# Optimization experiments

Hardware: AMD Instinct MI355X
Metric: run time of the kernel (lower is better)

## Reference

```python
import jax, jax.numpy as jnp
import numpy as np

B, S, H = 1, 2048, 2048
NH = 16
Q_LORA, KV_LORA = 1536, 512
D_NOPE, D_ROPE, D_V = 128, 64, 128
D_QK = D_NOPE + D_ROPE  # 192
EPS = 1e-6
ROPE_BASE = 10000.0


def setup_inputs() -> dict:
    key = jax.random.key(0)
    ks = jax.random.split(key, 8)
    def lin(k, fan_in, fan_out):
        # nn.Linear default init, stored as [in, out] for x @ W
        bound = 1.0 / np.sqrt(fan_in)
        return jax.random.uniform(k, (fan_in, fan_out), jnp.float32, -bound, bound)
    return {
        "hidden_states": jax.random.normal(ks[0], (B, S, H), jnp.float32),
        "Wqa": lin(ks[1], H, Q_LORA),
        "q_a_ln_w": jnp.ones((Q_LORA,), jnp.float32),
        "Wqb": lin(ks[2], Q_LORA, NH * D_QK),
        "Wkva": lin(ks[3], H, KV_LORA + D_ROPE),
        "kv_a_ln_w": jnp.ones((KV_LORA,), jnp.float32),
        "Wkvb": lin(ks[4], KV_LORA, NH * (D_NOPE + D_V)),
        "Wo": lin(ks[5], NH * D_V, H),
    }


def _rmsnorm(x, w):
    xf = x.astype(jnp.float32)
    var = jnp.mean(xf * xf, axis=-1, keepdims=True)
    return w * (xf * jax.lax.rsqrt(var + EPS)).astype(x.dtype)


def _rotate_half(x):
    x1, x2 = jnp.split(x, 2, axis=-1)
    return jnp.concatenate((-x2, x1), axis=-1)


def _rope_tables(seq_len, dtype=jnp.float32):
    inv_freq = 1.0 / (ROPE_BASE ** (jnp.arange(0, D_ROPE, 2, dtype=jnp.float32) / D_ROPE))
    t = jnp.arange(seq_len, dtype=jnp.float32)
    freqs = jnp.outer(t, inv_freq)                      # [S, D_ROPE/2]
    emb = jnp.concatenate((freqs, freqs), axis=-1)      # [S, D_ROPE]
    return jnp.cos(emb).astype(dtype), jnp.sin(emb).astype(dtype)


def reference(hidden_states, Wqa, q_a_ln_w, Wqb, Wkva, kv_a_ln_w, Wkvb, Wo):
    bsz, q_len, _ = hidden_states.shape
    scale = D_QK ** -0.5

    # Q path: LoRA down -> RMSNorm -> up
    q = _rmsnorm(hidden_states @ Wqa, q_a_ln_w) @ Wqb            # [B,S,NH*D_QK]
    q = q.reshape(bsz, q_len, NH, D_QK).transpose(0, 2, 1, 3)    # [B,NH,S,D_QK]
    q_nope, q_pe = q[..., :D_NOPE], q[..., D_NOPE:]

    # KV path: compressed latent + shared rope key
    ckv = hidden_states @ Wkva                                    # [B,S,KV_LORA+D_ROPE]
    compressed_kv, k_pe = ckv[..., :KV_LORA], ckv[..., KV_LORA:]
    k_pe = k_pe.reshape(bsz, q_len, 1, D_ROPE).transpose(0, 2, 1, 3)  # [B,1,S,D_ROPE]
    kv = _rmsnorm(compressed_kv, kv_a_ln_w) @ Wkvb                # [B,S,NH*(D_NOPE+D_V)]
    kv = kv.reshape(bsz, q_len, NH, D_NOPE + D_V).transpose(0, 2, 1, 3)
    k_nope, v = kv[..., :D_NOPE], kv[..., D_NOPE:]                # [B,NH,S,D_NOPE], [B,NH,S,D_V]

    # decoupled RoPE on the rope sub-dims
    cos, sin = _rope_tables(q_len, hidden_states.dtype)
    cos = cos[None, None]  # [1,1,S,D_ROPE] broadcast over batch & heads
    sin = sin[None, None]
    q_pe = q_pe * cos + _rotate_half(q_pe) * sin
    k_pe = k_pe * cos + _rotate_half(k_pe) * sin                  # [B,1,S,D_ROPE]

    query = jnp.concatenate([q_nope, q_pe], axis=-1)              # [B,NH,S,D_QK]
    key = jnp.concatenate([k_nope, jnp.broadcast_to(k_pe, (bsz, NH, q_len, D_ROPE))], axis=-1)

    attn = jnp.einsum('bhqd,bhkd->bhqk', query, key) * scale      # [B,NH,S,S]
    causal = jnp.triu(jnp.ones((q_len, q_len), bool), k=1)
    attn = jnp.where(causal, -jnp.inf, attn)
    attn = jax.nn.softmax(attn.astype(jnp.float32), axis=-1).astype(query.dtype)

    out = jnp.einsum('bhqk,bhkd->bhqd', attn, v)                  # [B,NH,S,D_V]
    out = out.transpose(0, 2, 1, 3).reshape(bsz, q_len, NH * D_V)
    return out @ Wo                                               # [B,S,H]
```

## Files before the change

kernel.cpp:

```cpp
#include <hip/hip_runtime.h>
#include <hip/hip_bf16.h>
#include <math.h>

#define S_LEN 2048
#define H_DIM 2048
#define NH 16
#define Q_LORA 1536
#define KV_LORA 512
#define D_NOPE 128
#define D_ROPE 64
#define D_V 128
#define D_QK 192

typedef unsigned short ushort_t;
typedef __attribute__((ext_vector_type(8))) short short8;
typedef __attribute__((ext_vector_type(4))) float f32x4;

__device__ __forceinline__ ushort_t f2bf(float f) {
    unsigned int u = __float_as_uint(f);
    u = (u + 0x7FFFu + ((u >> 16) & 1u)) >> 16;
    return (ushort_t)u;
}
__device__ __forceinline__ float bf2f(ushort_t u) {
    return __uint_as_float(((unsigned int)u) << 16);
}

__device__ __forceinline__ void storeC(float* p, float v) { *p = v; }
__device__ __forceinline__ void storeC(ushort_t* p, float v) { *p = f2bf(v); }

__device__ __forceinline__ void gload_lds16(const ushort_t* g, ushort_t* l) {
    __builtin_amdgcn_global_load_lds(
        (const __attribute__((address_space(1))) unsigned int*)(const void*)g,
        (__attribute__((address_space(3))) unsigned int*)(void*)l, 16, 0, 0);
}

__device__ __forceinline__ float dpp_max16(float x) {
    x = fmaxf(x, __int_as_float(__builtin_amdgcn_update_dpp(0, __float_as_int(x), 0xB1, 0xF, 0xF, true)));
    x = fmaxf(x, __int_as_float(__builtin_amdgcn_update_dpp(0, __float_as_int(x), 0x4E, 0xF, 0xF, true)));
    x = fmaxf(x, __int_as_float(__builtin_amdgcn_update_dpp(0, __float_as_int(x), 0x124, 0xF, 0xF, true)));
    x = fmaxf(x, __int_as_float(__builtin_amdgcn_update_dpp(0, __float_as_int(x), 0x128, 0xF, 0xF, true)));
    return x;
}
__device__ __forceinline__ float dpp_sum16(float x) {
    x += __int_as_float(__builtin_amdgcn_update_dpp(0, __float_as_int(x), 0xB1, 0xF, 0xF, true));
    x += __int_as_float(__builtin_amdgcn_update_dpp(0, __float_as_int(x), 0x4E, 0xF, 0xF, true));
    x += __int_as_float(__builtin_amdgcn_update_dpp(0, __float_as_int(x), 0x124, 0xF, 0xF, true));
    x += __int_as_float(__builtin_amdgcn_update_dpp(0, __float_as_int(x), 0x128, 0xF, 0xF, true));
    return x;
}

__device__ __forceinline__ void convT_body(
    const float* __restrict__ W, ushort_t* __restrict__ Wt,
    int K, int N, int n0, int k0, float (*tile)[33])
{
    const int tr = threadIdx.x >> 5, tc = threadIdx.x & 31;
    #pragma unroll
    for (int i = 0; i < 4; ++i) {
        int r = tr + i * 8;
        float v = 0.f;
        if (n0 + tc < N) v = W[(size_t)(k0 + r) * N + n0 + tc];
        tile[r][tc] = v;
    }
    __syncthreads();
    #pragma unroll
    for (int i = 0; i < 4; ++i) {
        int r = tr + i * 8;
        Wt[(size_t)(n0 + r) * K + k0 + tc] = f2bf(tile[tc][r]);
    }
}

__global__ __launch_bounds__(256) void unified_conv(
    const float* __restrict__ hs, ushort_t* __restrict__ hs16,
    const float* __restrict__ Wqa, const float* __restrict__ Wkva,
    const float* __restrict__ Wqb, const float* __restrict__ Wkvb,
    const float* __restrict__ Wo,
    ushort_t* __restrict__ WcatT, ushort_t* __restrict__ WqbT,
    ushort_t* __restrict__ WkvbT, ushort_t* __restrict__ WoT)
{
    __shared__ float tile[32][33];
    int b = blockIdx.x;
    if (b < 4096) {
        int base = (b * 256 + threadIdx.x) * 4;
        float4 v = *(const float4*)(hs + base);
        hs16[base + 0] = f2bf(v.x);
        hs16[base + 1] = f2bf(v.y);
        hs16[base + 2] = f2bf(v.z);
        hs16[base + 3] = f2bf(v.w);
        return;
    }
    b -= 4096;
    const float* W; ushort_t* Wt; int K, N, nbx;
    if (b < 3072)        {            W = Wqa;  Wt = WcatT;                              K = 2048; N = 1536; nbx = 48;  }
    else if (b < 4352)   { b -= 3072; W = Wkva; Wt = WcatT + (size_t)Q_LORA * H_DIM;     K = 2048; N = 576;  nbx = 20;  }
    else if (b < 8960)   { b -= 4352; W = Wqb;  Wt = WqbT;                               K = 1536; N = 3072; nbx = 96;  }
    else if (b < 11008)  { b -= 8960; W = Wkvb; Wt = WkvbT;                              K = 512;  N = 4096; nbx = 128; }
    else                 { b -= 11008; W = Wo;  Wt = WoT;                                K = 2048; N = 2048; nbx = 64;  }
    convT_body(W, Wt, K, N, (b % nbx) * 32, (b / nbx) * 32, tile);
}

__global__ __launch_bounds__(256) void fused_norm_ropek(
    const ushort_t* __restrict__ cat16r, ushort_t* __restrict__ qa16,
    ushort_t* __restrict__ ckv16n, ushort_t* __restrict__ kpe16,
    const float* __restrict__ qlnw, const float* __restrict__ klnw)
{
    __shared__ float red[4];
    const int b = blockIdx.x;
    if (b < 4096) {
        const bool isQ = (b < 2048);
        const int row = isQ ? b : b - 2048;
        const int K = isQ ? Q_LORA : KV_LORA;
        const ushort_t* x = cat16r + (size_t)row * 2176 + (isQ ? 0 : Q_LORA);
        ushort_t* y = (isQ ? qa16 + (size_t)row * Q_LORA : ckv16n + (size_t)row * KV_LORA);
        const float* wv = isQ ? qlnw : klnw;
        float ss = 0.f;
        for (int i = threadIdx.x; i < K; i += 256) { float v = bf2f(x[i]); ss += v * v; }
        #pragma unroll
        for (int off = 32; off > 0; off >>= 1) ss += __shfl_down(ss, off);
        int lane = threadIdx.x & 63, wid = threadIdx.x >> 6;
        if (lane == 0) red[wid] = ss;
        __syncthreads();
        float tot = red[0] + red[1] + red[2] + red[3];
        float rs = rsqrtf(tot / (float)K + 1e-6f);
        for (int i = threadIdx.x; i < K; i += 256)
            y[i] = f2bf(bf2f(x[i]) * rs * wv[i]);
    } else {
        int idx = (b - 4096) * 256 + threadIdx.x;
        if (idx >= S_LEN * 32) return;
        int i = idx & 31;
        int s = idx >> 5;
        float inv = powf(10000.0f, -(2.0f * i) / 64.0f);
        float ang = (float)s * inv;
        float c = cosf(ang), sn = sinf(ang);
        const ushort_t* p = cat16r + (size_t)s * 2176 + Q_LORA + KV_LORA;
        ushort_t* q = kpe16 + (size_t)s * D_ROPE;
        float x1 = bf2f(p[i]), x2 = bf2f(p[i + 32]);
        q[i]      = f2bf(x1 * c - x2 * sn);
        q[i + 32] = f2bf(x2 * c + x1 * sn);
    }
}

__global__ __launch_bounds__(256) void conv_vT_kernel(
    const ushort_t* __restrict__ kv, ushort_t* __restrict__ v16t)
{
    __shared__ ushort_t tile[32][33];
    const int h = blockIdx.z;
    const int s0 = blockIdx.x * 32, d0 = blockIdx.y * 32;
    const int tr = threadIdx.x >> 5, tc = threadIdx.x & 31;
    #pragma unroll
    for (int i = 0; i < 4; ++i) {
        int r = tr + i * 8;
        tile[r][tc] = kv[(size_t)(s0 + r) * 4096 + h * 256 + D_NOPE + d0 + tc];
    }
    __syncthreads();
    #pragma unroll
    for (int i = 0; i < 4; ++i) {
        int r = tr + i * 8;
        v16t[(size_t)h * D_V * S_LEN + (size_t)(d0 + r) * S_LEN + s0 + tc] = tile[tc][r];
    }
}

template <typename CT>
__device__ __forceinline__ void gemm_body_128(
    const ushort_t* __restrict__ A, const ushort_t* __restrict__ Bt,
    CT* __restrict__ C, int N, int K, int m0, int n0,
    ushort_t* Al, ushort_t* Bl)
{
    const int tid = threadIdx.x;
    const int lane = tid & 63;
    const int w = tid >> 6;
    const int lm = lane & 15, quad = lane >> 4;
    const int wr = w >> 1, wc = w & 1;

    f32x4 acc[4][4];
    #pragma unroll
    for (int a = 0; a < 4; ++a)
        #pragma unroll
        for (int b = 0; b < 4; ++b) acc[a][b] = (f32x4){0.f, 0.f, 0.f, 0.f};

    const int rrow = tid >> 2;
    const int rcol = (tid & 3) * 8;

    for (int k0 = 0; k0 < K; k0 += 64) {
        __syncthreads();
        #pragma unroll
        for (int c = 0; c < 2; ++c)
            #pragma unroll
            for (int half = 0; half < 2; ++half) {
                gload_lds16(A + (size_t)(m0 + half * 64 + rrow) * K + k0 + c * 32 + rcol,
                            Al + c * 4096 + half * 2048 + tid * 8);
                gload_lds16(Bt + (size_t)(n0 + half * 64 + rrow) * K + k0 + c * 32 + rcol,
                            Bl + c * 4096 + half * 2048 + tid * 8);
            }
        __syncthreads();

        #pragma unroll
        for (int c = 0; c < 2; ++c) {
            short8 af[4], bf[4];
            #pragma unroll
            for (int t = 0; t < 4; ++t)
                af[t] = *(const short8*)(Al + c * 4096 + (wr * 64 + t * 16 + lm) * 32 + quad * 8);
            #pragma unroll
            for (int t = 0; t < 4; ++t)
                bf[t] = *(const short8*)(Bl + c * 4096 + (wc * 64 + t * 16 + lm) * 32 + quad * 8);
            #pragma unroll
            for (int mt = 0; mt < 4; ++mt)
                #pragma unroll
                for (int nt = 0; nt < 4; ++nt)
                    acc[mt][nt] = __builtin_amdgcn_mfma_f32_16x16x32_bf16(
                        af[mt], bf[nt], acc[mt][nt], 0, 0, 0);
        }
    }

    #pragma unroll
    for (int mt = 0; mt < 4; ++mt)
        #pragma unroll
        for (int nt = 0; nt < 4; ++nt)
            #pragma unroll
            for (int r = 0; r < 4; ++r) {
                int row = m0 + wr * 64 + mt * 16 + quad * 4 + r;
                int col = n0 + wc * 64 + nt * 16 + lm;
                storeC(&C[(size_t)row * N + col], acc[mt][nt][r]);
            }
}

template <typename CT>
__global__ __launch_bounds__(256) void mfma_gemm_bt(
    const ushort_t* __restrict__ A, const ushort_t* __restrict__ Bt,
    CT* __restrict__ C, int N, int K)
{
    __shared__ ushort_t Al[2 * 128 * 32];
    __shared__ ushort_t Bl[2 * 128 * 32];
    gemm_body_128<CT>(A, Bt, C, N, K, blockIdx.y * 128, blockIdx.x * 128, Al, Bl);
}

__global__ __launch_bounds__(256) void mfma_gemm_dual(
    const ushort_t* __restrict__ A1, const ushort_t* __restrict__ Bt1,
    ushort_t* __restrict__ C1, int N1, int K1, int nb1,
    const ushort_t* __restrict__ A2, const ushort_t* __restrict__ Bt2,
    ushort_t* __restrict__ C2, int N2, int K2)
{
    __shared__ ushort_t Al[2 * 128 * 32];
    __shared__ ushort_t Bl[2 * 128 * 32];
    int g = blockIdx.x;
    if (g < nb1) {
        int nbx = N1 / 128;
        gemm_body_128<ushort_t>(A1, Bt1, C1, N1, K1, (g / nbx) * 128, (g % nbx) * 128, Al, Bl);
    } else {
        g -= nb1;
        int nbx = N2 / 128;
        gemm_body_128<ushort_t>(A2, Bt2, C2, N2, K2, (g / nbx) * 128, (g % nbx) * 128, Al, Bl);
    }
}

__device__ __forceinline__ void softmax_step(
    f32x4 s[4], int k0, int qw, int lm, int quad,
    float m_[4], float l_[4], f32x4 O[8], ushort_t* ps)
{
    const float scale = 0.07216878364870322f;
    #pragma unroll
    for (int r = 0; r < 4; ++r) {
        int qrow = qw + quad * 4 + r;
        float a[4];
        #pragma unroll
        for (int st = 0; st < 4; ++st)
            a[st] = (k0 + st * 16 + lm <= qrow) ? s[st][r] * scale : -1e30f;
        float mx = dpp_max16(fmaxf(fmaxf(a[0], a[1]), fmaxf(a[2], a[3])));
        float mn = fmaxf(m_[r], mx);
        float p[4];
        #pragma unroll
        for (int st = 0; st < 4; ++st) p[st] = __expf(a[st] - mn);
        float alpha = __expf(m_[r] - mn);
        float psum = dpp_sum16((p[0] + p[1]) + (p[2] + p[3]));
        l_[r] = l_[r] * alpha + psum;
        m_[r] = mn;
        #pragma unroll
        for (int c = 0; c < 8; ++c) O[c][r] *= alpha;
        #pragma unroll
        for (int st = 0; st < 4; ++st)
            ps[(quad * 4 + r) * 72 + st * 16 + lm] = f2bf(p[st]);
    }
}

__global__ __launch_bounds__(128) void mla_attn_kernel(
    const ushort_t* __restrict__ qb, const ushort_t* __restrict__ kvb,
    const ushort_t* __restrict__ kpe, const ushort_t* __restrict__ v16t,
    ushort_t* __restrict__ aout16)
{
    __shared__ ushort_t Kn[4 * 64 * 32];
    __shared__ ushort_t Kr[2 * 64 * 32];
    __shared__ ushort_t Vt[2 * 128 * 32];
    __shared__ ushort_t Ps[2][16][72];

    const int h = blockIdx.x;
    const int q0 = 32 * (63 - blockIdx.y);
    const int w = threadIdx.x >> 6;
    const int lane = threadIdx.x & 63;
    const int lm = lane & 15, quad = lane >> 4;
    const int qw = q0 + 16 * w;
    ushort_t* myPs = &Ps[w][0][0];

    const int skey = lane >> 2;
    const int ssw  = ((lane & 3) ^ ((lane >> 3) & 3)) * 8;
    const int swq  = quad ^ ((lm >> 1) & 3);

    short8 qf[6];
    #pragma unroll
    for (int f = 0; f < 6; ++f)
        qf[f] = *(const short8*)(qb + (size_t)(qw + lm) * 3072 + h * 192 + f * 32 + quad * 8);
    {
        float srow = (float)(qw + lm);
        #pragma unroll
        for (int j = 0; j < 8; ++j) {
            int i = quad * 8 + j;
            float inv = powf(10000.0f, -(2.0f * i) / 64.0f);
            float ang = srow * inv;
            float c = cosf(ang), sn = sinf(ang);
            float x1 = bf2f((ushort_t)qf[4][j]);
            float x2 = bf2f((ushort_t)qf[5][j]);
            qf[4][j] = (short)f2bf(x1 * c - x2 * sn);
            qf[5][j] = (short)f2bf(x2 * c + x1 * sn);
        }
    }

    f32x4 O[8];
    #pragma unroll
    for (int c = 0; c < 8; ++c) O[c] = (f32x4){0.f, 0.f, 0.f, 0.f};
    float m_[4] = {-1e30f, -1e30f, -1e30f, -1e30f};
    float l_[4] = {0.f, 0.f, 0.f, 0.f};

    const int kend = q0 + 32;
    for (int k0 = 0; k0 < kend; k0 += 64) {
        __syncthreads();
        {
            #pragma unroll
            for (int fi = 0; fi < 2; ++fi) {
                int f = 2 * w + fi;
                #pragma unroll
                for (int i = 0; i < 4; ++i)
                    gload_lds16(kvb + (size_t)(k0 + i * 16 + skey) * 4096 + h * 256 + f * 32 + ssw,
                                Kn + f * 2048 + i * 512 + lane * 8);
            }
            #pragma unroll
            for (int i = 0; i < 4; ++i)
                gload_lds16(kpe + (size_t)(k0 + i * 16 + skey) * 64 + w * 32 + ssw,
                            Kr + w * 2048 + i * 512 + lane * 8);
            #pragma unroll
            for (int j = 0; j < 8; ++j)
                gload_lds16(v16t + ((size_t)h * 128 + j * 16 + skey) * S_LEN + k0 + w * 32 + ssw,
                            Vt + w * 4096 + j * 512 + lane * 8);
        }
        __syncthreads();

        if (k0 < qw + 16) {
            f32x4 s[4];
            #pragma unroll
            for (int st = 0; st < 4; ++st) s[st] = (f32x4){0.f, 0.f, 0.f, 0.f};
            __builtin_amdgcn_s_setprio(1);
            #pragma unroll
            for (int f = 0; f < 4; ++f)
                #pragma unroll
                for (int st = 0; st < 4; ++st) {
                    short8 kf = *(const short8*)(Kn + f * 2048 + (st * 16 + lm) * 32 + swq * 8);
                    s[st] = __builtin_amdgcn_mfma_f32_16x16x32_bf16(qf[f], kf, s[st], 0, 0, 0);
                }
            #pragma unroll
            for (int f2 = 0; f2 < 2; ++f2)
                #pragma unroll
                for (int st = 0; st < 4; ++st) {
                    short8 kf = *(const short8*)(Kr + f2 * 2048 + (st * 16 + lm) * 32 + swq * 8);
                    s[st] = __builtin_amdgcn_mfma_f32_16x16x32_bf16(qf[4 + f2], kf, s[st], 0, 0, 0);
                }
            __builtin_amdgcn_s_setprio(0);

            softmax_step(s, k0, qw, lm, quad, m_, l_, O, myPs);

            asm volatile("s_waitcnt lgkmcnt(0)" ::: "memory");
            short8 pf0 = *(const short8*)(myPs + lm * 72 + quad * 8);
            short8 pf1 = *(const short8*)(myPs + lm * 72 + 32 + quad * 8);
            __builtin_amdgcn_s_setprio(1);
            #pragma unroll
            for (int c = 0; c < 8; ++c) {
                short8 vf0 = *(const short8*)(Vt + (c * 16 + lm) * 32 + swq * 8);
                short8 vf1 = *(const short8*)(Vt + 4096 + (c * 16 + lm) * 32 + swq * 8);
                O[c] = __builtin_amdgcn_mfma_f32_16x16x32_bf16(pf0, vf0, O[c], 0, 0, 0);
                O[c] = __builtin_amdgcn_mfma_f32_16x16x32_bf16(pf1, vf1, O[c], 0, 0, 0);
            }
            __builtin_amdgcn_s_setprio(0);
        }
    }
    #pragma unroll
    for (int c = 0; c < 8; ++c)
        #pragma unroll
        for (int r = 0; r < 4; ++r) {
            int qrow = qw + quad * 4 + r;
            aout16[(size_t)qrow * 2048 + h * D_V + c * 16 + lm] = f2bf(O[c][r] / l_[r]);
        }
}

extern "C" void kernel_launch(void* const* d_in, const int* in_sizes, int n_in,
                              void* d_out, int out_size, void* d_ws, size_t ws_size,
                              hipStream_t stream)
{
    (void)in_sizes; (void)n_in; (void)out_size; (void)ws_size;
    const float* hs   = (const float*)d_in[0];
    const float* Wqa  = (const float*)d_in[1];
    const float* qlnw = (const float*)d_in[2];
    const float* Wqb  = (const float*)d_in[3];
    const float* Wkva = (const float*)d_in[4];
    const float* klnw = (const float*)d_in[5];
    const float* Wkvb = (const float*)d_in[6];
    const float* Wo   = (const float*)d_in[7];
    float* out = (float*)d_out;

    ushort_t* p = (ushort_t*)d_ws;
    ushort_t* hs16   = p; p += (size_t)S_LEN * H_DIM;
    ushort_t* WcatT  = p; p += (size_t)2176 * H_DIM;
    ushort_t* WqbT   = p; p += (size_t)3072 * Q_LORA;
    ushort_t* WkvbT  = p; p += (size_t)4096 * KV_LORA;
    ushort_t* WoT    = p; p += (size_t)H_DIM * H_DIM;
    ushort_t* cat16r = p; p += (size_t)S_LEN * 2176;
    ushort_t* qa16   = p; p += (size_t)S_LEN * Q_LORA;
    ushort_t* qbuf16 = p; p += (size_t)S_LEN * 3072;
    ushort_t* ckv16n = p; p += (size_t)S_LEN * KV_LORA;
    ushort_t* kpe16  = p; p += (size_t)S_LEN * D_ROPE;
    ushort_t* kv16   = p; p += (size_t)S_LEN * 4096;
    ushort_t* v16t   = p; p += (size_t)NH * D_V * S_LEN;
    ushort_t* aout16 = p; p += (size_t)S_LEN * 2048;

    unified_conv<<<19200, 256, 0, stream>>>(
        hs, hs16, Wqa, Wkva, Wqb, Wkvb, Wo, WcatT, WqbT, WkvbT, WoT);
    mfma_gemm_bt<ushort_t><<<dim3(2176 / 128, S_LEN / 128), 256, 0, stream>>>(
        hs16, WcatT, cat16r, 2176, H_DIM);
    fused_norm_ropek<<<4096 + 256, 256, 0, stream>>>(cat16r, qa16, ckv16n, kpe16, qlnw, klnw);
    mfma_gemm_dual<<<384 + 512, 256, 0, stream>>>(
        qa16, WqbT, qbuf16, 3072, Q_LORA, 384,
        ckv16n, WkvbT, kv16, 4096, KV_LORA);
    conv_vT_kernel<<<dim3(S_LEN / 32, D_V / 32, NH), 256, 0, stream>>>(kv16, v16t);
    mla_attn_kernel<<<dim3(NH, 64), 128, 0, stream>>>(qbuf16, kv16, kpe16, v16t, aout16);
    mfma_gemm_bt<float><<<dim3(H_DIM / 128, S_LEN / 128), 256, 0, stream>>>(
        aout16, WoT, out, H_DIM, H_DIM);
}
```

Before: 347.5 us.

## Double-buffer GEMM LDS tiles with swizzle and widen attention blocks to 64 queries

After: 340.6 us. -2.0%, faster.

```diff
diff --git a/kernel.cpp b/kernel.cpp
--- a/kernel.cpp
+++ b/kernel.cpp
@@ -178,30 +178,43 @@
         for (int b = 0; b < 4; ++b) acc[a][b] = (f32x4){0.f, 0.f, 0.f, 0.f};
 
     const int rrow = tid >> 2;
-    const int rcol = (tid & 3) * 8;
-
-    for (int k0 = 0; k0 < K; k0 += 64) {
-        __syncthreads();
+    const int rcsw = ((tid & 3) ^ ((tid >> 3) & 3)) * 8;
+    const int swq  = quad ^ ((lm >> 1) & 3);
+
+    const int NT = K >> 6;
+
+    auto stage = [&](int buf, int k0) {
         #pragma unroll
         for (int c = 0; c < 2; ++c)
             #pragma unroll
             for (int half = 0; half < 2; ++half) {
-                gload_lds16(A + (size_t)(m0 + half * 64 + rrow) * K + k0 + c * 32 + rcol,
-                            Al + c * 4096 + half * 2048 + tid * 8);
-                gload_lds16(Bt + (size_t)(n0 + half * 64 + rrow) * K + k0 + c * 32 + rcol,
-                            Bl + c * 4096 + half * 2048 + tid * 8);
-            }
-        __syncthreads();
-
+                gload_lds16(A + (size_t)(m0 + half * 64 + rrow) * K + k0 + c * 32 + rcsw,
+                            Al + buf * 8192 + c * 4096 + half * 2048 + tid * 8);
+                gload_lds16(Bt + (size_t)(n0 + half * 64 + rrow) * K + k0 + c * 32 + rcsw,
+                            Bl + buf * 8192 + c * 4096 + half * 2048 + tid * 8);
+            }
+    };
+
+    stage(0, 0);
+    asm volatile("s_waitcnt vmcnt(0)" ::: "memory");
+    __builtin_amdgcn_s_barrier();
+    __builtin_amdgcn_sched_barrier(0);
+
+    int cur = 0;
+    for (int t = 0; t < NT; ++t) {
+        if (t + 1 < NT) stage(cur ^ 1, (t + 1) << 6);
+
+        const ushort_t* Ab = Al + cur * 8192;
+        const ushort_t* Bb = Bl + cur * 8192;
         #pragma unroll
         for (int c = 0; c < 2; ++c) {
             short8 af[4], bf[4];
             #pragma unroll
-            for (int t = 0; t < 4; ++t)
-                af[t] = *(const short8*)(Al + c * 4096 + (wr * 64 + t * 16 + lm) * 32 + quad * 8);
-            #pragma unroll
-            for (int t = 0; t < 4; ++t)
-                bf[t] = *(const short8*)(Bl + c * 4096 + (wc * 64 + t * 16 + lm) * 32 + quad * 8);
+            for (int t2 = 0; t2 < 4; ++t2)
+                af[t2] = *(const short8*)(Ab + c * 4096 + (wr * 64 + t2 * 16 + lm) * 32 + swq * 8);
+            #pragma unroll
+            for (int t2 = 0; t2 < 4; ++t2)
+                bf[t2] = *(const short8*)(Bb + c * 4096 + (wc * 64 + t2 * 16 + lm) * 32 + swq * 8);
             #pragma unroll
             for (int mt = 0; mt < 4; ++mt)
                 #pragma unroll
@@ -209,6 +222,11 @@
                     acc[mt][nt] = __builtin_amdgcn_mfma_f32_16x16x32_bf16(
                         af[mt], bf[nt], acc[mt][nt], 0, 0, 0);
         }
+
+        asm volatile("s_waitcnt vmcnt(0)" ::: "memory");
+        __builtin_amdgcn_s_barrier();
+        __builtin_amdgcn_sched_barrier(0);
+        cur ^= 1;
     }
 
     #pragma unroll
@@ -228,8 +246,8 @@
     const ushort_t* __restrict__ A, const ushort_t* __restrict__ Bt,
     CT* __restrict__ C, int N, int K)
 {
-    __shared__ ushort_t Al[2 * 128 * 32];
-    __shared__ ushort_t Bl[2 * 128 * 32];
+    __shared__ ushort_t Al[2 * 8192];
+    __shared__ ushort_t Bl[2 * 8192];
     gemm_body_128<CT>(A, Bt, C, N, K, blockIdx.y * 128, blockIdx.x * 128, Al, Bl);
 }
 
@@ -239,8 +257,8 @@
     const ushort_t* __restrict__ A2, const ushort_t* __restrict__ Bt2,
     ushort_t* __restrict__ C2, int N2, int K2)
 {
-    __shared__ ushort_t Al[2 * 128 * 32];
-    __shared__ ushort_t Bl[2 * 128 * 32];
+    __shared__ ushort_t Al[2 * 8192];
+    __shared__ ushort_t Bl[2 * 8192];
     int g = blockIdx.x;
     if (g < nb1) {
         int nbx = N1 / 128;
@@ -281,7 +299,7 @@
     }
 }
 
-__global__ __launch_bounds__(128) void mla_attn_kernel(
+__global__ __launch_bounds__(256) void mla_attn_kernel(
     const ushort_t* __restrict__ qb, const ushort_t* __restrict__ kvb,
     const ushort_t* __restrict__ kpe, const ushort_t* __restrict__ v16t,
     ushort_t* __restrict__ aout16)
@@ -289,15 +307,15 @@
     __shared__ ushort_t Kn[4 * 64 * 32];
     __shared__ ushort_t Kr[2 * 64 * 32];
     __shared__ ushort_t Vt[2 * 128 * 32];
-    __shared__ ushort_t Ps[2][16][72];
+    __shared__ ushort_t Ps[4][16 * 72];
 
     const int h = blockIdx.x;
-    const int q0 = 32 * (63 - blockIdx.y);
+    const int q0 = 64 * (31 - blockIdx.y);
     const int w = threadIdx.x >> 6;
     const int lane = threadIdx.x & 63;
     const int lm = lane & 15, quad = lane >> 4;
     const int qw = q0 + 16 * w;
-    ushort_t* myPs = &Ps[w][0][0];
+    ushort_t* myPs = Ps[w];
 
     const int skey = lane >> 2;
     const int ssw  = ((lane & 3) ^ ((lane >> 3) & 3)) * 8;
@@ -328,64 +346,58 @@
     float m_[4] = {-1e30f, -1e30f, -1e30f, -1e30f};
     float l_[4] = {0.f, 0.f, 0.f, 0.f};
 
-    const int kend = q0 + 32;
+    const int kend = q0 + 64;
     for (int k0 = 0; k0 < kend; k0 += 64) {
         __syncthreads();
         {
             #pragma unroll
-            for (int fi = 0; fi < 2; ++fi) {
-                int f = 2 * w + fi;
-                #pragma unroll
-                for (int i = 0; i < 4; ++i)
-                    gload_lds16(kvb + (size_t)(k0 + i * 16 + skey) * 4096 + h * 256 + f * 32 + ssw,
-                                Kn + f * 2048 + i * 512 + lane * 8);
-            }
-            #pragma unroll
             for (int i = 0; i < 4; ++i)
-                gload_lds16(kpe + (size_t)(k0 + i * 16 + skey) * 64 + w * 32 + ssw,
-                            Kr + w * 2048 + i * 512 + lane * 8);
-            #pragma unroll
-            for (int j = 0; j < 8; ++j)
-                gload_lds16(v16t + ((size_t)h * 128 + j * 16 + skey) * S_LEN + k0 + w * 32 + ssw,
-                            Vt + w * 4096 + j * 512 + lane * 8);
+                gload_lds16(kvb + (size_t)(k0 + i * 16 + skey) * 4096 + h * 256 + w * 32 + ssw,
+                            Kn + w * 2048 + i * 512 + lane * 8);
+            #pragma unroll
+            for (int ii = 0; ii < 2; ++ii) {
+                int i = 2 * (w & 1) + ii;
+                gload_lds16(kpe + (size_t)(k0 + i * 16 + skey) * 64 + (w >> 1) * 32 + ssw,
+                            Kr + (w >> 1) * 2048 + i * 512 + lane * 8);
+            }
+            #pragma unroll
+            for (int jj = 0; jj < 4; ++jj) {
+                int j = 4 * (w >> 1) + jj;
+                gload_lds16(v16t + ((size_t)h * 128 + j * 16 + skey) * S_LEN + k0 + (w & 1) * 32 + ssw,
+                            Vt + (w & 1) * 4096 + j * 512 + lane * 8);
+            }
         }
         __syncthreads();
 
-        if (k0 < qw + 16) {
-            f32x4 s[4];
-            #pragma unroll
-            for (int st = 0; st < 4; ++st) s[st] = (f32x4){0.f, 0.f, 0.f, 0.f};
-            __builtin_amdgcn_s_setprio(1);
-            #pragma unroll
-            for (int f = 0; f < 4; ++f)
-                #pragma unroll
-                for (int st = 0; st < 4; ++st) {
-                    short8 kf = *(const short8*)(Kn + f * 2048 + (st * 16 + lm) * 32 + swq * 8);
-                    s[st] = __builtin_amdgcn_mfma_f32_16x16x32_bf16(qf[f], kf, s[st], 0, 0, 0);
-                }
-            #pragma unroll
-            for (int f2 = 0; f2 < 2; ++f2)
-                #pragma unroll
-                for (int st = 0; st < 4; ++st) {
-                    short8 kf = *(const short8*)(Kr + f2 * 2048 + (st * 16 + lm) * 32 + swq * 8);
-                    s[st] = __builtin_amdgcn_mfma_f32_16x16x32_bf16(qf[4 + f2], kf, s[st], 0, 0, 0);
-                }
-            __builtin_amdgcn_s_setprio(0);
-
-            softmax_step(s, k0, qw, lm, quad, m_, l_, O, myPs);
-
-            asm volatile("s_waitcnt lgkmcnt(0)" ::: "memory");
-            short8 pf0 = *(const short8*)(myPs + lm * 72 + quad * 8);
-            short8 pf1 = *(const short8*)(myPs + lm * 72 + 32 + quad * 8);
-            __builtin_amdgcn_s_setprio(1);
-            #pragma unroll
-            for (int c = 0; c < 8; ++c) {
-                short8 vf0 = *(const short8*)(Vt + (c * 16 + lm) * 32 + swq * 8);
-                short8 vf1 = *(const short8*)(Vt + 4096 + (c * 16 + lm) * 32 + swq * 8);
-                O[c] = __builtin_amdgcn_mfma_f32_16x16x32_bf16(pf0, vf0, O[c], 0, 0, 0);
-                O[c] = __builtin_amdgcn_mfma_f32_16x16x32_bf16(pf1, vf1, O[c], 0, 0, 0);
-            }
-            __builtin_amdgcn_s_setprio(0);
+        f32x4 s[4];
+        #pragma unroll
+        for (int st = 0; st < 4; ++st) s[st] = (f32x4){0.f, 0.f, 0.f, 0.f};
+        #pragma unroll
+        for (int f = 0; f < 4; ++f)
+            #pragma unroll
+            for (int st = 0; st < 4; ++st) {
+                short8 kf = *(const short8*)(Kn + f * 2048 + (st * 16 + lm) * 32 + swq * 8);
+                s[st] = __builtin_amdgcn_mfma_f32_16x16x32_bf16(qf[f], kf, s[st], 0, 0, 0);
+            }
+        #pragma unroll
+        for (int f2 = 0; f2 < 2; ++f2)
+            #pragma unroll
+            for (int st = 0; st < 4; ++st) {
+                short8 kf = *(const short8*)(Kr + f2 * 2048 + (st * 16 + lm) * 32 + swq * 8);
+                s[st] = __builtin_amdgcn_mfma_f32_16x16x32_bf16(qf[4 + f2], kf, s[st], 0, 0, 0);
+            }
+
+        softmax_step(s, k0, qw, lm, quad, m_, l_, O, myPs);
+
+        asm volatile("s_waitcnt lgkmcnt(0)" ::: "memory");
+        short8 pf0 = *(const short8*)(myPs + lm * 72 + quad * 8);
+        short8 pf1 = *(const short8*)(myPs + lm * 72 + 32 + quad * 8);
+        #pragma unroll
+        for (int c = 0; c < 8; ++c) {
+            short8 vf0 = *(const short8*)(Vt + (c * 16 + lm) * 32 + swq * 8);
+            short8 vf1 = *(const short8*)(Vt + 4096 + (c * 16 + lm) * 32 + swq * 8);
+            O[c] = __builtin_amdgcn_mfma_f32_16x16x32_bf16(pf0, vf0, O[c], 0, 0, 0);
+            O[c] = __builtin_amdgcn_mfma_f32_16x16x32_bf16(pf1, vf1, O[c], 0, 0, 0);
         }
     }
     #pragma unroll
@@ -436,7 +448,7 @@
         qa16, WqbT, qbuf16, 3072, Q_LORA, 384,
         ckv16n, WkvbT, kv16, 4096, KV_LORA);
     conv_vT_kernel<<<dim3(S_LEN / 32, D_V / 32, NH), 256, 0, stream>>>(kv16, v16t);
-    mla_attn_kernel<<<dim3(NH, 64), 128, 0, stream>>>(qbuf16, kv16, kpe16, v16t, aout16);
+    mla_attn_kernel<<<dim3(NH, 32), 256, 0, stream>>>(qbuf16, kv16, kpe16, v16t, aout16);
     mfma_gemm_bt<float><<<dim3(H_DIM / 128, S_LEN / 128), 256, 0, stream>>>(
         aout16, WoT, out, H_DIM, H_DIM);
 }
```
